# Kernel tuning notes

Hardware: AMD Instinct MI355X
Metric: run time of the kernel (lower is better)

The kernel has to match this reference:

```python
import jax, jax.numpy as jnp
import numpy as np

SCALE = 64.0
MARGIN = 0.5
ALPHA = 1.2
SIGMA = 2.0
THRESH = float(np.cos(np.pi - MARGIN))
MM = float(np.sin(np.pi - MARGIN) * MARGIN)
IN_F, OUT_F, BATCH = 512, 100000, 512


def setup_inputs() -> dict:
    key = jax.random.key(0)
    k1, k2, k3 = jax.random.split(key, 3)
    x = jax.random.normal(k1, (BATCH, IN_F), dtype=jnp.float32)
    label = jax.random.randint(k2, (BATCH,), 0, OUT_F, dtype=jnp.int64 if jax.config.read('jax_enable_x64') else jnp.int32)
    stdv = 1.0 / np.sqrt(IN_F)
    weight = jax.random.uniform(k3, (OUT_F, IN_F), dtype=jnp.float32, minval=-stdv, maxval=stdv)
    return {"input": x, "label": label, "weight": weight}


def reference(input, label, weight):
    # row-normalize embeddings and class weights
    ex = input / jnp.linalg.norm(input, axis=1, keepdims=True)
    ew = weight / jnp.linalg.norm(weight, axis=1, keepdims=True)
    cos = jnp.einsum('bd,cd->bc', ex, ew)  # [B, C]

    b = jnp.arange(cos.shape[0])
    cos_lb = cos[b, label]  # [B] cosine at the true class
    # arcface margin: cos(theta + m) above thresh, linear fallback below
    target = jnp.where(cos_lb > THRESH,
                       jnp.cos(jnp.arccos(cos_lb) + MARGIN),
                       cos_lb - MM)  # [B]

    # negative reweighting: gaussian around the margined target (detached)
    t_scale = ALPHA * jnp.exp(-jnp.square(cos - target[:, None]) / SIGMA)
    t_scale = jax.lax.stop_gradient(t_scale)

    onehot = jax.nn.one_hot(label, cos.shape[1], dtype=cos.dtype)  # a_scale; c_scale = 1 - onehot
    logits = SCALE * (onehot * target[:, None]
                      + (1.0 - onehot) * (t_scale * cos + t_scale - 1.0))
    return logits
```

## Files before the change

kernel.cpp:

```cpp
#include <hip/hip_runtime.h>
#include <hip/hip_bf16.h>

typedef unsigned short ushort_t;
typedef unsigned int uint_t;

typedef __attribute__((ext_vector_type(8))) short short8;
typedef __attribute__((ext_vector_type(4))) float f32x4;

#define BATCH 512
#define DK    512
#define CTOT  100000
#define BN    32
#define THRESH_C (-0.8775825618903728f)
#define MM_C     (0.2397127693021015f)

static __device__ __forceinline__ ushort_t f2bf(float f) {
    union { float f; uint_t u; } v; v.f = f;
    return (ushort_t)((v.u + 0x7FFFu + ((v.u >> 16) & 1u)) >> 16);
}

__global__ __launch_bounds__(256) void arc_prep(
    const float* __restrict__ x, const int* __restrict__ label,
    const float* __restrict__ w, float* __restrict__ target,
    ushort_t* __restrict__ exbF)
{
    const int b = blockIdx.x;
    const int t = threadIdx.x;
    __shared__ float red[8];

    const float2 xv = ((const float2*)(x + (size_t)b * DK))[t];
    float ss = xv.x * xv.x + xv.y * xv.y;
    #pragma unroll
    for (int o = 32; o; o >>= 1) ss += __shfl_xor(ss, o);
    if ((t & 63) == 0) red[t >> 6] = ss;
    __syncthreads();
    const float ssx = red[0] + red[1] + red[2] + red[3];
    const float rnx = 1.0f / sqrtf(ssx);

    {
        const int k = 2 * t;
        const int ko = k >> 5;
        const int qk = (k >> 3) & 3;
        const int kj = k & 7;
        const size_t F = (size_t)(b >> 4) * 8192 + (size_t)ko * 512
                       + (size_t)qk * 128 + (size_t)(b & 15) * 8 + kj;
        ushort2 e;
        e.x = f2bf(xv.x * rnx);
        e.y = f2bf(xv.y * rnx);
        *(ushort2*)(exbF + F) = e;
    }

    const int lb = label[b];
    const float2 wv = ((const float2*)(w + (size_t)lb * DK))[t];
    float ssw = wv.x * wv.x + wv.y * wv.y;
    float dot = xv.x * wv.x + xv.y * wv.y;
    #pragma unroll
    for (int o = 32; o; o >>= 1) { ssw += __shfl_xor(ssw, o); dot += __shfl_xor(dot, o); }
    __syncthreads();
    if ((t & 63) == 0) { red[t >> 6] = ssw; red[4 + (t >> 6)] = dot; }
    __syncthreads();
    if (t == 0) {
        const float sw = red[0] + red[1] + red[2] + red[3];
        const float dt = red[4] + red[5] + red[6] + red[7];
        float cl = dt * rnx / sqrtf(sw);
        cl = fminf(fmaxf(cl, -1.0f), 1.0f);
        const float tg = (cl > THRESH_C) ? cosf(acosf(cl) + 0.5f) : (cl - MM_C);
        target[b] = tg;
    }
}

__global__ __launch_bounds__(256) void arc_wcvt(
    const float* __restrict__ w, ushort_t* __restrict__ wbF,
    float* __restrict__ rnw)
{
    const int rb  = blockIdx.x;
    const int t   = threadIdx.x;
    const int r   = t >> 4;
    const int c16 = t & 15;
    const int row = rb * 16 + r;
    const float* wrow = w + (size_t)row * DK;
    ushort_t* fbase = wbF + (size_t)rb * 8192 + (size_t)r * 8;

    float ss = 0.0f;
    #pragma unroll
    for (int i = 0; i < 8; ++i) {
        const int c = i * 64 + c16 * 4;
        const float4 q = *(const float4*)(wrow + c);
        ss += q.x * q.x + q.y * q.y + q.z * q.z + q.w * q.w;
        ushort4 e;
        e.x = f2bf(q.x); e.y = f2bf(q.y); e.z = f2bf(q.z); e.w = f2bf(q.w);
        const int ko = c >> 5;
        const int qk = (c >> 3) & 3;
        const int j0 = c & 7;
        *(ushort4*)(fbase + ko * 512 + qk * 128 + j0) = e;
    }
    ss += __shfl_xor(ss, 1);
    ss += __shfl_xor(ss, 2);
    ss += __shfl_xor(ss, 4);
    ss += __shfl_xor(ss, 8);
    if (c16 == 0) rnw[row] = 1.0f / sqrtf(ss);
}

__global__ __launch_bounds__(256, 6) void arc_main_ff(
    const ushort_t* __restrict__ exbF, const ushort_t* __restrict__ wbF,
    const float* __restrict__ rnw, const int* __restrict__ label,
    const float* __restrict__ target, float* __restrict__ out)
{
    const int t    = threadIdx.x;
    const int lane = t & 63;
    const int tile = blockIdx.x >> 1;
    const int rg   = (t >> 6) + 4 * (blockIdx.x & 1);
    const int c0   = tile * BN;
    const int colq = lane & 15;
    const int qk   = lane >> 4;

    const ushort_t* abase = exbF + (size_t)(rg * 4) * 8192 + (size_t)lane * 8;
    const ushort_t* bbase = wbF + (size_t)(tile * 2) * 8192 + (size_t)lane * 8;

    f32x4 acc[4][2];
    #pragma unroll
    for (int i = 0; i < 4; ++i)
        #pragma unroll
        for (int j = 0; j < 2; ++j)
            acc[i][j] = (f32x4){0.f, 0.f, 0.f, 0.f};

    #pragma unroll 4
    for (int ko = 0; ko < 16; ++ko) {
        const short8 b0 = *(const short8*)(bbase + ko * 512);
        const short8 b1 = *(const short8*)(bbase + 8192 + ko * 512);
        #pragma unroll
        for (int mt = 0; mt < 4; ++mt) {
            const short8 afr = *(const short8*)(abase + (size_t)mt * 8192 + ko * 512);
            acc[mt][0] = __builtin_amdgcn_mfma_f32_16x16x32_bf16(afr, b0, acc[mt][0], 0, 0, 0);
            acc[mt][1] = __builtin_amdgcn_mfma_f32_16x16x32_bf16(afr, b1, acc[mt][1], 0, 0, 0);
        }
    }

    const float rn0 = rnw[c0 + colq];
    const float rn1 = rnw[c0 + 16 + colq];

    const int m0 = rg * 64;
    #pragma unroll
    for (int mt = 0; mt < 4; ++mt) {
        #pragma unroll
        for (int rr = 0; rr < 4; ++rr) {
            const int row = m0 + mt * 16 + qk * 4 + rr;
            const float tg = target[row];
            const int   lb = label[row];
            float* orow = out + (size_t)row * CTOT + c0;
            {
                const float cosv = acc[mt][0][rr] * rn0;
                const float d  = cosv - tg;
                const float ts = 1.2f * __expf(d * d * -0.5f);
                const float v  = ((c0 + colq) == lb) ? 64.0f * tg
                                                     : 64.0f * (ts * cosv + ts - 1.0f);
                __builtin_nontemporal_store(v, &orow[colq]);
            }
            {
                const float cosv = acc[mt][1][rr] * rn1;
                const float d  = cosv - tg;
                const float ts = 1.2f * __expf(d * d * -0.5f);
                const float v  = ((c0 + 16 + colq) == lb) ? 64.0f * tg
                                                          : 64.0f * (ts * cosv + ts - 1.0f);
                __builtin_nontemporal_store(v, &orow[16 + colq]);
            }
        }
    }
}

__global__ __launch_bounds__(512, 8) void arc_main_lds(
    const ushort_t* __restrict__ exbF, const float* __restrict__ w,
    const int* __restrict__ label, const float* __restrict__ target,
    float* __restrict__ out)
{
    __shared__ ushort_t Bs[BN * DK];

    const int t    = threadIdx.x;
    const int lane = t & 63;
    const int wid  = t >> 6;
    const int c0   = blockIdx.x * BN;

    const int br  = t >> 4;
    const int bj  = t & 15;
    const float* wrow = w + (size_t)(c0 + br) * DK;
    const int s3 = br & 7;
    float bsq = 0.0f;
    #pragma unroll
    for (int i = 0; i < 8; ++i) {
        const int c = i * 64 + bj * 4;
        const float4 q = *(const float4*)(wrow + c);
        bsq += q.x * q.x + q.y * q.y + q.z * q.z + q.w * q.w;
        uint2 p;
        p.x = (uint_t)f2bf(q.x) | ((uint_t)f2bf(q.y) << 16);
        p.y = (uint_t)f2bf(q.z) | ((uint_t)f2bf(q.w) << 16);
        const int k16 = c >> 3;
        const int sw  = k16 ^ s3;
        *(uint2*)&Bs[br * DK + sw * 8 + (bj & 1) * 4] = p;
    }
    bsq += __shfl_xor(bsq, 1);
    bsq += __shfl_xor(bsq, 2);
    bsq += __shfl_xor(bsq, 4);
    bsq += __shfl_xor(bsq, 8);
    __syncthreads();

    const int m0   = wid * 64;
    const int colq = lane & 15;
    const int qk   = lane >> 4;
    const int bs3  = colq & 7;
    const ushort_t* abase = exbF + (size_t)(wid * 4) * 8192 + (size_t)lane * 8;

    f32x4 acc[4][2];
    #pragma unroll
    for (int i = 0; i < 4; ++i)
        #pragma unroll
        for (int j = 0; j < 2; ++j)
            acc[i][j] = (f32x4){0.f, 0.f, 0.f, 0.f};

    #pragma unroll 2
    for (int ko = 0; ko < 16; ++ko) {
        short8 bfr[2];
        #pragma unroll
        for (int nt = 0; nt < 2; ++nt) {
            const int idx = (nt * 16 + colq) * DK + (((ko << 2) | qk) ^ bs3) * 8;
            bfr[nt] = *(const short8*)&Bs[idx];
        }
        #pragma unroll
        for (int mt = 0; mt < 4; ++mt) {
            const short8 afr = *(const short8*)(abase + (size_t)mt * 8192 + ko * 512);
            acc[mt][0] = __builtin_amdgcn_mfma_f32_16x16x32_bf16(afr, bfr[0], acc[mt][0], 0, 0, 0);
            acc[mt][1] = __builtin_amdgcn_mfma_f32_16x16x32_bf16(afr, bfr[1], acc[mt][1], 0, 0, 0);
        }
    }

    __syncthreads();
    if (bj == 0) ((float*)Bs)[br] = 1.0f / sqrtf(bsq);
    __syncthreads();
    float rn[2];
    rn[0] = ((float*)Bs)[colq];
    rn[1] = ((float*)Bs)[16 + colq];

    #pragma unroll
    for (int mt = 0; mt < 4; ++mt) {
        #pragma unroll
        for (int rr = 0; rr < 4; ++rr) {
            const int row = m0 + mt * 16 + qk * 4 + rr;
            const float tg = target[row];
            const int   lb = label[row];
            float* orow = out + (size_t)row * CTOT + c0;
            #pragma unroll
            for (int nt = 0; nt < 2; ++nt) {
                const int cc = c0 + nt * 16 + colq;
                const float cosv = acc[mt][nt][rr] * rn[nt];
                const float d  = cosv - tg;
                const float ts = 1.2f * __expf(d * d * -0.5f);
                const float v  = (cc == lb) ? 64.0f * tg
                                            : 64.0f * (ts * cosv + ts - 1.0f);
                orow[nt * 16 + colq] = v;
            }
        }
    }
}

extern "C" void kernel_launch(void* const* d_in, const int* in_sizes, int n_in,
                              void* d_out, int out_size, void* d_ws, size_t ws_size,
                              hipStream_t stream) {
    const float* x     = (const float*)d_in[0];
    const int*   label = (const int*)d_in[1];
    const float* w     = (const float*)d_in[2];
    float* out = (float*)d_out;

    float*    target = (float*)d_ws;
    ushort_t* exbF   = (ushort_t*)((char*)d_ws + 2048);
    float*    rnw    = (float*)((char*)d_ws + 526336);
    ushort_t* wbF    = (ushort_t*)((char*)d_ws + 935936);
    const size_t WS_NEED = 935936 + (size_t)CTOT * DK * 2;

    arc_prep<<<512, 256, 0, stream>>>(x, label, w, target, exbF);

    if (ws_size >= WS_NEED) {
        arc_wcvt<<<CTOT / 16, 256, 0, stream>>>(w, wbF, rnw);
        arc_main_ff<<<(CTOT / BN) * 2, 256, 0, stream>>>(exbF, wbF, rnw, label, target, out);
    } else {
        arc_main_lds<<<CTOT / BN, 512, 0, stream>>>(exbF, w, label, target, out);
    }
}
```

Measured before the change: 449.0 us.

## Widen main kernel tile to 64 columns with 512-thread blocks and padded weights

```diff
diff --git a/kernel.cpp b/kernel.cpp
--- a/kernel.cpp
+++ b/kernel.cpp
@@ -10,7 +10,9 @@
 #define BATCH 512
 #define DK    512
 #define CTOT  100000
+#define CPAD  100032
 #define BN    32
+#define BNF   64
 #define THRESH_C (-0.8775825618903728f)
 #define MM_C     (0.2397127693021015f)
 
@@ -78,94 +80,111 @@
     const int r   = t >> 4;
     const int c16 = t & 15;
     const int row = rb * 16 + r;
+    const bool valid = (row < CTOT);
     const float* wrow = w + (size_t)row * DK;
     ushort_t* fbase = wbF + (size_t)rb * 8192 + (size_t)r * 8;
 
     float ss = 0.0f;
     #pragma unroll
-    for (int i = 0; i < 8; ++i) {
-        const int c = i * 64 + c16 * 4;
-        const float4 q = *(const float4*)(wrow + c);
-        ss += q.x * q.x + q.y * q.y + q.z * q.z + q.w * q.w;
-        ushort4 e;
-        e.x = f2bf(q.x); e.y = f2bf(q.y); e.z = f2bf(q.z); e.w = f2bf(q.w);
+    for (int i = 0; i < 4; ++i) {
+        const int c = i * 128 + c16 * 8;
+        float4 q0 = make_float4(0.f, 0.f, 0.f, 0.f);
+        float4 q1 = q0;
+        if (valid) {
+            q0 = *(const float4*)(wrow + c);
+            q1 = *(const float4*)(wrow + c + 4);
+        }
+        ss += q0.x * q0.x + q0.y * q0.y + q0.z * q0.z + q0.w * q0.w
+            + q1.x * q1.x + q1.y * q1.y + q1.z * q1.z + q1.w * q1.w;
+        uint4 p;
+        p.x = (uint_t)f2bf(q0.x) | ((uint_t)f2bf(q0.y) << 16);
+        p.y = (uint_t)f2bf(q0.z) | ((uint_t)f2bf(q0.w) << 16);
+        p.z = (uint_t)f2bf(q1.x) | ((uint_t)f2bf(q1.y) << 16);
+        p.w = (uint_t)f2bf(q1.z) | ((uint_t)f2bf(q1.w) << 16);
         const int ko = c >> 5;
         const int qk = (c >> 3) & 3;
-        const int j0 = c & 7;
-        *(ushort4*)(fbase + ko * 512 + qk * 128 + j0) = e;
+        *(uint4*)(fbase + ko * 512 + qk * 128) = p;
     }
     ss += __shfl_xor(ss, 1);
     ss += __shfl_xor(ss, 2);
     ss += __shfl_xor(ss, 4);
     ss += __shfl_xor(ss, 8);
-    if (c16 == 0) rnw[row] = 1.0f / sqrtf(ss);
-}
-
-__global__ __launch_bounds__(256, 6) void arc_main_ff(
+    if (c16 == 0) rnw[row] = valid ? (1.0f / sqrtf(ss)) : 0.0f;
+}
+
+__global__ __launch_bounds__(512, 4) void arc_main_ff(
     const ushort_t* __restrict__ exbF, const ushort_t* __restrict__ wbF,
     const float* __restrict__ rnw, const int* __restrict__ label,
     const float* __restrict__ target, float* __restrict__ out)
 {
     const int t    = threadIdx.x;
     const int lane = t & 63;
-    const int tile = blockIdx.x >> 1;
-    const int rg   = (t >> 6) + 4 * (blockIdx.x & 1);
-    const int c0   = tile * BN;
+    const int wid  = t >> 6;
+    const int tile = blockIdx.x;
+    const int c0   = tile * BNF;
     const int colq = lane & 15;
     const int qk   = lane >> 4;
 
-    const ushort_t* abase = exbF + (size_t)(rg * 4) * 8192 + (size_t)lane * 8;
-    const ushort_t* bbase = wbF + (size_t)(tile * 2) * 8192 + (size_t)lane * 8;
-
-    f32x4 acc[4][2];
+    const ushort_t* abase = exbF + (size_t)(wid * 4) * 8192 + (size_t)lane * 8;
+    const ushort_t* bbase = wbF + (size_t)(tile * 4) * 8192 + (size_t)lane * 8;
+
+    f32x4 acc[4][4];
     #pragma unroll
     for (int i = 0; i < 4; ++i)
         #pragma unroll
-        for (int j = 0; j < 2; ++j)
+        for (int j = 0; j < 4; ++j)
             acc[i][j] = (f32x4){0.f, 0.f, 0.f, 0.f};
 
     #pragma unroll 4
     for (int ko = 0; ko < 16; ++ko) {
-        const short8 b0 = *(const short8*)(bbase + ko * 512);
-        const short8 b1 = *(const short8*)(bbase + 8192 + ko * 512);
+        short8 bfr[4];
+        #pragma unroll
+        for (int nt = 0; nt < 4; ++nt)
+            bfr[nt] = *(const short8*)(bbase + (size_t)nt * 8192 + ko * 512);
         #pragma unroll
         for (int mt = 0; mt < 4; ++mt) {
             const short8 afr = *(const short8*)(abase + (size_t)mt * 8192 + ko * 512);
-            acc[mt][0] = __builtin_amdgcn_mfma_f32_16x16x32_bf16(afr, b0, acc[mt][0], 0, 0, 0);
-            acc[mt][1] = __builtin_amdgcn_mfma_f32_16x16x32_bf16(afr, b1, acc[mt][1], 0, 0, 0);
-        }
-    }
-
-    const float rn0 = rnw[c0 + colq];
-    const float rn1 = rnw[c0 + 16 + colq];
-
-    const int m0 = rg * 64;
-    #pragma unroll
-    for (int mt = 0; mt < 4; ++mt) {
-        #pragma unroll
-        for (int rr = 0; rr < 4; ++rr) {
-            const int row = m0 + mt * 16 + qk * 4 + rr;
-            const float tg = target[row];
-            const int   lb = label[row];
-            float* orow = out + (size_t)row * CTOT + c0;
-            {
-                const float cosv = acc[mt][0][rr] * rn0;
-                const float d  = cosv - tg;
-                const float ts = 1.2f * __expf(d * d * -0.5f);
-                const float v  = ((c0 + colq) == lb) ? 64.0f * tg
-                                                     : 64.0f * (ts * cosv + ts - 1.0f);
-                __builtin_nontemporal_store(v, &orow[colq]);
-            }
-            {
-                const float cosv = acc[mt][1][rr] * rn1;
-                const float d  = cosv - tg;
-                const float ts = 1.2f * __expf(d * d * -0.5f);
-                const float v  = ((c0 + 16 + colq) == lb) ? 64.0f * tg
-                                                          : 64.0f * (ts * cosv + ts - 1.0f);
-                __builtin_nontemporal_store(v, &orow[16 + colq]);
-            }
-        }
-    }
+            #pragma unroll
+            for (int nt = 0; nt < 4; ++nt)
+                acc[mt][nt] = __builtin_amdgcn_mfma_f32_16x16x32_bf16(afr, bfr[nt], acc[mt][nt], 0, 0, 0);
+        }
+    }
+
+    float rn[4];
+    #pragma unroll
+    for (int nt = 0; nt < 4; ++nt) rn[nt] = rnw[c0 + nt * 16 + colq];
+
+    const int m0 = wid * 64;
+
+#define EPILOGUE(GUARD)                                                        \
+    _Pragma("unroll")                                                          \
+    for (int mt = 0; mt < 4; ++mt) {                                           \
+        _Pragma("unroll")                                                      \
+        for (int rr = 0; rr < 4; ++rr) {                                       \
+            const int row = m0 + mt * 16 + qk * 4 + rr;                        \
+            const float tg = target[row];                                      \
+            const int   lb = label[row];                                       \
+            float* orow = out + (size_t)row * CTOT + c0;                       \
+            _Pragma("unroll")                                                  \
+            for (int nt = 0; nt < 4; ++nt) {                                   \
+                const int cc = c0 + nt * 16 + colq;                            \
+                if (GUARD && cc >= CTOT) continue;                             \
+                const float cosv = acc[mt][nt][rr] * rn[nt];                   \
+                const float d  = cosv - tg;                                    \
+                const float ts = 1.2f * __expf(d * d * -0.5f);                 \
+                const float v  = (cc == lb) ? 64.0f * tg                       \
+                                            : 64.0f * (ts * cosv + ts - 1.0f); \
+                __builtin_nontemporal_store(v, &orow[nt * 16 + colq]);         \
+            }                                                                  \
+        }                                                                      \
+    }
+
+    if (c0 + BNF <= CTOT) {
+        EPILOGUE(false)
+    } else {
+        EPILOGUE(true)
+    }
+#undef EPILOGUE
 }
 
 __global__ __launch_bounds__(512, 8) void arc_main_lds(
@@ -272,14 +291,14 @@
     float*    target = (float*)d_ws;
     ushort_t* exbF   = (ushort_t*)((char*)d_ws + 2048);
     float*    rnw    = (float*)((char*)d_ws + 526336);
-    ushort_t* wbF    = (ushort_t*)((char*)d_ws + 935936);
-    const size_t WS_NEED = 935936 + (size_t)CTOT * DK * 2;
+    ushort_t* wbF    = (ushort_t*)((char*)d_ws + 926720);
+    const size_t WS_NEED = 926720 + (size_t)CPAD * DK * 2;
 
     arc_prep<<<512, 256, 0, stream>>>(x, label, w, target, exbF);
 
     if (ws_size >= WS_NEED) {
-        arc_wcvt<<<CTOT / 16, 256, 0, stream>>>(w, wbF, rnw);
-        arc_main_ff<<<(CTOT / BN) * 2, 256, 0, stream>>>(exbF, wbF, rnw, label, target, out);
+        arc_wcvt<<<CPAD / 16, 256, 0, stream>>>(w, wbF, rnw);
+        arc_main_ff<<<CPAD / BNF, 512, 0, stream>>>(exbF, wbF, rnw, label, target, out);
     } else {
         arc_main_lds<<<CTOT / BN, 512, 0, stream>>>(exbF, w, label, target, out);
     }
```

Result: no change. 451.1 us (+0.5%).
